# Kernel tuning notes

Measured on AMD Instinct MI355X. Metric: run time of the kernel, lower is better.

The kernel has to match this reference:

```python
import jax, jax.numpy as jnp
import numpy as np


def setup_inputs() -> dict:
    key = jax.random.key(0)
    ks = jax.random.split(key, 24)
    Bz, L, D, U, A, K, V, E, QW = 64, 2048, 512, 512, 512, 64, 32000, 256, 7
    s = 0.02  # weight scale to keep tanh/sigmoid/softmax in a sane range

    def n(k, shape, scale):
        return jax.random.normal(k, shape, dtype=jnp.float32) * scale

    return dict(
        prev_target=n(ks[0], (Bz, V), 0.05),
        prev_hidden=n(ks[1], (Bz, U), 0.05),
        features=n(ks[2], (Bz, L, D), 1.0),
        Bmat=n(ks[3], (Bz, L, 1), 1.0),
        Wa=n(ks[4], (U, A), s),
        Ua=n(ks[5], (D, A), s),
        Va=n(ks[6], (A, 1), s),
        Uf=n(ks[7], (K, A), s),
        Qk=n(ks[8], (QW, 1, K), s),   # Conv1D kernel (W, in_ch=1, out_ch=k)
        We=n(ks[9], (V, E), s),
        Wccz=n(ks[10], (D, U), s),
        Wyz=n(ks[11], (E, U), s),
        Uhz=n(ks[12], (U, U), s),
        Wyr=n(ks[13], (E, U), s),
        Uhr=n(ks[14], (U, U), s),
        Ccr=n(ks[15], (D, U), s),
        Wyh=n(ks[16], (E, U), s),
        b_wyh=jnp.zeros((U,), dtype=jnp.float32),
        Urh=n(ks[17], (U, U), s),
        b_urh=jnp.zeros((U,), dtype=jnp.float32),
        Wo=n(ks[18], (E, V), s),
        Wh=n(ks[19], (U, E), s),
        Wc=n(ks[20], (D, E), s),
    )


def reference(prev_target, prev_hidden, features, Bmat, Wa, Ua, Va, Uf, Qk,
              We, Wccz, Wyz, Uhz, Wyr, Uhr, Ccr, Wyh, b_wyh, Urh, b_urh,
              Wo, Wh, Wc):
    # --- AttentionMLP ---
    # Conv1D(filters=k, kernel_size=q_width, padding='same'), B: (b, L, 1) -> F: (b, L, k)
    F = jax.lax.conv_general_dilated(
        Bmat, Qk, window_strides=(1,), padding='SAME',
        dimension_numbers=('NWC', 'WIO', 'NWC'))
    # e: (b, L, A) = Wa h[:,None,:] + Ua features + Uf F
    e = (prev_hidden @ Wa)[:, None, :] + features @ Ua + F @ Uf
    e = jnp.tanh(e) @ Va                      # (b, L, 1)
    attn = jax.nn.softmax(e, axis=1)          # softmax over L (the reshape trick)
    context = jnp.sum(attn * features, axis=1)  # (b, D)

    # --- GRU-style gating ---
    Ey = prev_target @ We                     # (b, E)
    ccz = context @ Wccz                      # (b, U)
    zt = jax.nn.sigmoid(Ey @ Wyz + prev_hidden @ Uhz + ccz)
    rt = jax.nn.sigmoid(Ey @ Wyr + prev_hidden @ Uhr + context @ Ccr)
    h_cand = jnp.tanh(Ey @ Wyh + b_wyh + (rt * prev_hidden) @ Urh + b_urh + ccz)
    ht = (1.0 - zt) * prev_hidden + zt * h_cand

    # --- Output projection ---
    out = Ey + ht @ Wh + context @ Wc         # (b, E)
    out = jax.nn.softmax(out @ Wo, axis=-1)   # (b, V)
    return out, ht, attn
```

## Files before the change

kernel.cpp:

```cpp
#include <hip/hip_runtime.h>
#include <hip/hip_bf16.h>

typedef unsigned short u16;
typedef __attribute__((ext_vector_type(4))) float f32x4;
typedef __attribute__((ext_vector_type(8))) short bf16x8;

#define BZ 64
#define LSEQ 2048
#define DDIM 512
#define UDIM 512
#define ADIM 512
#define VOC 32000
#define EDIM 256

__device__ __forceinline__ u16 f2bf(float f) {
    union { float f; unsigned int u; } v; v.f = f;
    unsigned int u = v.u;
    return (u16)((u + 0x7FFFu + ((u >> 16) & 1u)) >> 16);
}

__device__ __forceinline__ float fast_tanh(float x) {
    x = fminf(fmaxf(x, -15.f), 15.f);
    float e = __expf(2.f * x);
    return (e - 1.f) * __frcp_rn(e + 1.f);
}

__device__ __forceinline__ void stage16(const u16* __restrict__ g, u16* l, int lane) {
    *(uint4*)(l + lane * 8) = *(const uint4*)g;
}

__global__ void zero_k(float4* p, int n) {
    int i = blockIdx.x * 256 + threadIdx.x;
    if (i < n) { float4 z; z.x = z.y = z.z = z.w = 0.f; p[i] = z; }
}

#define MAXTJ 16
struct TJob { const float* src; u16* dst; int R, C, ld, tileEnd; };
struct TArgs { TJob j[MAXTJ]; int nj; };

__global__ __launch_bounds__(256) void transpose_pack(TArgs a) {
    __shared__ float ts[32][33];
    int bid = blockIdx.x;
    int ji = 0;
    while (bid >= a.j[ji].tileEnd) ji++;
    int tstart = ji ? a.j[ji - 1].tileEnd : 0;
    int local = bid - tstart;
    TJob J = a.j[ji];
    int tilesC = J.C >> 5;
    int tr = local / tilesC, tc = local - tr * tilesC;
    int r0 = tr << 5, c0 = tc << 5;
    int t = threadIdx.x, col = t & 31, row0 = t >> 5;
    #pragma unroll
    for (int i = 0; i < 4; i++) {
        int r = row0 + i * 8;
        ts[r][col] = J.src[(size_t)(r0 + r) * J.C + c0 + col];
    }
    __syncthreads();
    #pragma unroll
    for (int i = 0; i < 4; i++) {
        int crow = row0 + i * 8;
        J.dst[(size_t)(c0 + crow) * J.ld + r0 + col] = f2bf(ts[col][crow]);
    }
}

__global__ void pack_misc(const float* __restrict__ pt, const float* __restrict__ ph,
                          u16* __restrict__ ptb, u16* __restrict__ phb) {
    int idx = blockIdx.x * 256 + threadIdx.x;
    if (idx < BZ * VOC) ptb[idx] = f2bf(pt[idx]);
    int i2 = idx - BZ * VOC;
    if (i2 >= 0 && i2 < BZ * UDIM) phb[i2] = f2bf(ph[i2]);
}

__global__ __launch_bounds__(256) void prep_feat_k(
    const float* __restrict__ feat, const float* __restrict__ Bm,
    const float* __restrict__ Qk, u16* __restrict__ featbf)
{
    __shared__ float qs[448];
    __shared__ float bwin[72];
    int t = threadIdx.x;
    int row0 = blockIdx.x * 64;
    int b = row0 >> 11, l0 = row0 & 2047;
    if (t < 448) qs[t] = Qk[t];
    if (t < 70) { int l = l0 - 3 + t; bwin[t] = (l >= 0 && l < LSEQ) ? Bm[b * LSEQ + l] : 0.f; }
    __syncthreads();
    #pragma unroll
    for (int it = 0; it < 8; it++) {
        int r = it * 8 + (t >> 5), c = (t & 31) * 16;
        const float* p = feat + (size_t)(row0 + r) * DDIM + c;
        float4 a0 = *(const float4*)p, a1 = *(const float4*)(p + 4),
               a2 = *(const float4*)(p + 8), a3 = *(const float4*)(p + 12);
        u16 u[16] = { f2bf(a0.x), f2bf(a0.y), f2bf(a0.z), f2bf(a0.w),
                      f2bf(a1.x), f2bf(a1.y), f2bf(a1.z), f2bf(a1.w),
                      f2bf(a2.x), f2bf(a2.y), f2bf(a2.z), f2bf(a2.w),
                      f2bf(a3.x), f2bf(a3.y), f2bf(a3.z), f2bf(a3.w) };
        u16* dst = featbf + (size_t)(row0 + r) * 576 + c;
        *(uint4*)dst = *(uint4*)u;
        *(uint4*)(dst + 8) = *(uint4*)(u + 8);
    }
    {
        int r = t >> 2, c = (t & 3) * 16;
        float s[16];
        #pragma unroll
        for (int j = 0; j < 16; j++) s[j] = 0.f;
        #pragma unroll
        for (int w7 = 0; w7 < 7; w7++) {
            float bv = bwin[r + w7];
            #pragma unroll
            for (int j = 0; j < 16; j++) s[j] += bv * qs[w7 * 64 + c + j];
        }
        u16 u[16];
        #pragma unroll
        for (int j = 0; j < 16; j++) u[j] = f2bf(s[j]);
        u16* dst = featbf + (size_t)(row0 + r) * 576 + 512 + c;
        *(uint4*)dst = *(uint4*)u;
        *(uint4*)(dst + 8) = *(uint4*)(u + 8);
    }
}

#define MAXGJ 4
struct GJob { const u16* A; const u16* Bt; float* C;
              int ldA, ldB, ldC, nT, ckPer, ckTot, tileEnd, store; };
struct GArgs { GJob j[MAXGJ]; };

__global__ __launch_bounds__(256) void gemm_batch_k(GArgs ga) {
    __shared__ u16 As[64 * 32];
    __shared__ u16 Bs[64 * 32];
    int bid = blockIdx.x, ji = 0;
    while (bid >= ga.j[ji].tileEnd) ji++;
    GJob J = ga.j[ji];
    int local = bid - (ji ? ga.j[ji - 1].tileEnd : 0);
    int nti = local % J.nT, ksi = local / J.nT;
    int n0 = nti * 64;
    int ck0 = ksi * J.ckPer;
    int ckEnd = ck0 + J.ckPer; if (ckEnd > J.ckTot) ckEnd = J.ckTot;
    int tid = threadIdx.x, w = tid >> 6, lane = tid & 63, q = lane >> 4, cc = lane & 15;
    int wrow = lane >> 2, wseg = lane & 3;
    f32x4 acc[4];
    #pragma unroll
    for (int mt = 0; mt < 4; mt++) acc[mt] = (f32x4)0.f;
    const u16* Ab = J.A + (size_t)(w * 16 + wrow) * J.ldA + wseg * 8;
    const u16* Bb = J.Bt + (size_t)(n0 + w * 16 + wrow) * J.ldB + wseg * 8;
    for (int ck = ck0; ck < ckEnd; ck++) {
        int k0 = ck * 32;
        stage16(Ab + k0, &As[w * 512], lane);
        stage16(Bb + k0, &Bs[w * 512], lane);
        __syncthreads();
        bf16x8 af[4];
        #pragma unroll
        for (int mt = 0; mt < 4; mt++)
            af[mt] = *(const bf16x8*)&As[(mt * 16 + cc) * 32 + q * 8];
        bf16x8 bfr = *(const bf16x8*)&Bs[(w * 16 + cc) * 32 + q * 8];
        #pragma unroll
        for (int mt = 0; mt < 4; mt++)
            acc[mt] = __builtin_amdgcn_mfma_f32_16x16x32_bf16(af[mt], bfr, acc[mt], 0, 0, 0);
        __syncthreads();
    }
    #pragma unroll
    for (int mt = 0; mt < 4; mt++) {
        #pragma unroll
        for (int rr = 0; rr < 4; rr++) {
            int m = mt * 16 + q * 4 + rr, n = n0 + w * 16 + cc;
            float v = acc[mt][rr];
            if (J.store) J.C[(size_t)m * J.ldC + n] = v;
            else atomicAdd(&J.C[(size_t)m * J.ldC + n], v);
        }
    }
}

__global__ __launch_bounds__(256) void attn_gemm_k(
    const u16* __restrict__ featbf, const u16* __restrict__ Wt,
    const float* __restrict__ hWa, const float* __restrict__ Va,
    float* __restrict__ e)
{
    __shared__ u16 As[128 * 32];
    __shared__ u16 Bs[128 * 32];
    int row0 = blockIdx.x * 128;
    int col0 = blockIdx.y * 128;
    int b = row0 >> 11;
    int tid = threadIdx.x, w = tid >> 6, lane = tid & 63, q = lane >> 4, cc = lane & 15;
    int wrow = lane >> 2, wseg = lane & 3;
    int rh = w & 1, ch = w >> 1;
    f32x4 acc[4][4];
    #pragma unroll
    for (int mt = 0; mt < 4; mt++)
        #pragma unroll
        for (int nt = 0; nt < 4; nt++) acc[mt][nt] = (f32x4)0.f;
    const u16* Abase = featbf + (size_t)row0 * 576 + wseg * 8;
    const u16* Bbase = Wt + (size_t)col0 * 576 + wseg * 8;
    for (int ck = 0; ck < 18; ck++) {
        int k0 = ck * 32;
        #pragma unroll
        for (int i = 0; i < 2; i++) {
            int rr = (i * 4 + w) * 16 + wrow;
            stage16(Abase + (size_t)rr * 576 + k0, &As[(i * 4 + w) * 512], lane);
            stage16(Bbase + (size_t)rr * 576 + k0, &Bs[(i * 4 + w) * 512], lane);
        }
        __syncthreads();
        bf16x8 af[4], bfr[4];
        #pragma unroll
        for (int mt = 0; mt < 4; mt++)
            af[mt] = *(const bf16x8*)&As[(rh * 64 + mt * 16 + cc) * 32 + q * 8];
        #pragma unroll
        for (int nt = 0; nt < 4; nt++)
            bfr[nt] = *(const bf16x8*)&Bs[(ch * 64 + nt * 16 + cc) * 32 + q * 8];
        #pragma unroll
        for (int mt = 0; mt < 4; mt++)
            #pragma unroll
            for (int nt = 0; nt < 4; nt++)
                acc[mt][nt] = __builtin_amdgcn_mfma_f32_16x16x32_bf16(af[mt], bfr[nt], acc[mt][nt], 0, 0, 0);
        __syncthreads();
    }
    float hv[4], vv[4];
    #pragma unroll
    for (int nt = 0; nt < 4; nt++) {
        int n = col0 + ch * 64 + nt * 16 + cc;
        hv[nt] = hWa[b * ADIM + n];
        vv[nt] = Va[n];
    }
    #pragma unroll
    for (int mt = 0; mt < 4; mt++) {
        #pragma unroll
        for (int rr = 0; rr < 4; rr++) {
            float s = 0.f;
            #pragma unroll
            for (int nt = 0; nt < 4; nt++)
                s += fast_tanh(hv[nt] + acc[mt][nt][rr]) * vv[nt];
            s += __shfl_xor(s, 1, 16);
            s += __shfl_xor(s, 2, 16);
            s += __shfl_xor(s, 4, 16);
            s += __shfl_xor(s, 8, 16);
            if (cc == 0)
                atomicAdd(&e[row0 + rh * 64 + mt * 16 + q * 4 + rr], s);
        }
    }
}

__global__ __launch_bounds__(256) void softmaxL_k(const float* __restrict__ e,
                                                  float* __restrict__ attn_ws,
                                                  float* __restrict__ attn_out) {
    int b = blockIdx.x, t = threadIdx.x;
    __shared__ float sm[4], ss[4];
    float v[8];
    float mx = -1e30f;
    #pragma unroll
    for (int i = 0; i < 8; i++) { v[i] = e[b * LSEQ + t + i * 256]; mx = fmaxf(mx, v[i]); }
    for (int o = 32; o; o >>= 1) mx = fmaxf(mx, __shfl_xor(mx, o, 64));
    if ((t & 63) == 0) sm[t >> 6] = mx;
    __syncthreads();
    mx = fmaxf(fmaxf(sm[0], sm[1]), fmaxf(sm[2], sm[3]));
    float s = 0.f;
    #pragma unroll
    for (int i = 0; i < 8; i++) { v[i] = __expf(v[i] - mx); s += v[i]; }
    for (int o = 32; o; o >>= 1) s += __shfl_xor(s, o, 64);
    if ((t & 63) == 0) ss[t >> 6] = s;
    __syncthreads();
    s = ss[0] + ss[1] + ss[2] + ss[3];
    float inv = 1.f / s;
    #pragma unroll
    for (int i = 0; i < 8; i++) {
        float p = v[i] * inv;
        attn_ws[b * LSEQ + t + i * 256] = p;
        attn_out[b * LSEQ + t + i * 256] = p;
    }
}

__global__ __launch_bounds__(256) void context2_k(
    const u16* __restrict__ featbf, const float* __restrict__ attn,
    float* __restrict__ ctx)
{
    __shared__ float at[256];
    int t = threadIdx.x, b = blockIdx.y, lc = blockIdx.x;
    at[t] = attn[b * LSEQ + lc * 256 + t];
    __syncthreads();
    int col = t * 2;
    const u16* base = featbf + (size_t)(b * LSEQ + lc * 256) * 576 + col;
    float a0 = 0.f, a1 = 0.f;
    #pragma unroll 4
    for (int l = 0; l < 256; l++) {
        unsigned int u = *(const unsigned int*)(base + (size_t)l * 576);
        union { unsigned int i; float f; } lo, hi;
        lo.i = u << 16; hi.i = u & 0xffff0000u;
        float av = at[l];
        a0 += av * lo.f;
        a1 += av * hi.f;
    }
    atomicAdd(&ctx[b * UDIM + col], a0);
    atomicAdd(&ctx[b * UDIM + col + 1], a1);
}

__global__ void pack_acat1_k(const float* __restrict__ Ey, const float* __restrict__ h,
                             const float* __restrict__ ctx, u16* __restrict__ Acat1,
                             const float* __restrict__ bwyh, const float* __restrict__ burh,
                             float* __restrict__ bsum) {
    int b = blockIdx.x, t = threadIdx.x;
    for (int col = t; col < 1280; col += 256) {
        float v = (col < 256) ? Ey[b * 256 + col]
                : (col < 768) ? h[b * 512 + col - 256]
                              : ctx[b * 512 + col - 768];
        Acat1[b * 1280 + col] = f2bf(v);
    }
    if (b == 0) { for (int i = t; i < 512; i += 256) bsum[i] = bwyh[i] + burh[i]; }
}

__global__ void pack_acath_k(const float* __restrict__ Ey, const float* __restrict__ rtp,
                             const float* __restrict__ h, u16* __restrict__ AcatH) {
    int b = blockIdx.x, t = threadIdx.x;
    for (int col = t; col < 768; col += 256) {
        float v;
        if (col < 256) v = Ey[b * 256 + col];
        else {
            int u = col - 256;
            float rt = 1.f / (1.f + __expf(-rtp[b * 512 + u]));
            v = rt * h[b * 512 + u];
        }
        AcatH[b * 768 + col] = f2bf(v);
    }
}

__global__ void pack_ht3_k(const float* __restrict__ ztp, const float* __restrict__ hcp,
                           const float* __restrict__ ccz, const float* __restrict__ bsum,
                           const float* __restrict__ h, const float* __restrict__ ctx,
                           float* __restrict__ ht_out, u16* __restrict__ Acat3) {
    int b = blockIdx.x, t = threadIdx.x;
    for (int u = t; u < 512; u += 256) {
        float z = 1.f / (1.f + __expf(-ztp[b * 512 + u]));
        float hcv = tanhf(hcp[b * 512 + u] + ccz[b * 512 + u] + bsum[u]);
        float v = (1.f - z) * h[b * 512 + u] + z * hcv;
        ht_out[b * 512 + u] = v;
        Acat3[b * 1024 + u] = f2bf(v);
        Acat3[b * 1024 + 512 + u] = f2bf(ctx[b * 512 + u]);
    }
}

__global__ void pack_G_k(const float* __restrict__ Gf32, const float* __restrict__ Ey,
                         u16* __restrict__ Gbf) {
    int b = blockIdx.x, t = threadIdx.x;
    Gbf[b * 256 + t] = f2bf(Gf32[b * 256 + t] + Ey[b * 256 + t]);
}

__global__ __launch_bounds__(1024) void softmaxV_k(const float* __restrict__ logits,
                                                   float* __restrict__ out) {
    int b = blockIdx.x, t = threadIdx.x;
    __shared__ float sm[16], ss[16];
    const float* lp = logits + (size_t)b * VOC;
    float mx = -1e30f;
    for (int i = t; i < VOC; i += 1024) mx = fmaxf(mx, lp[i]);
    for (int o = 32; o; o >>= 1) mx = fmaxf(mx, __shfl_xor(mx, o, 64));
    if ((t & 63) == 0) sm[t >> 6] = mx;
    __syncthreads();
    if (t < 16) {
        float m2 = sm[t];
        for (int o = 8; o; o >>= 1) m2 = fmaxf(m2, __shfl_xor(m2, o, 16));
        sm[t] = m2;
    }
    __syncthreads();
    mx = sm[0];
    float s = 0.f;
    for (int i = t; i < VOC; i += 1024) s += __expf(lp[i] - mx);
    for (int o = 32; o; o >>= 1) s += __shfl_xor(s, o, 64);
    if ((t & 63) == 0) ss[t >> 6] = s;
    __syncthreads();
    if (t < 16) {
        float s2 = ss[t];
        for (int o = 8; o; o >>= 1) s2 += __shfl_xor(s2, o, 16);
        ss[t] = s2;
    }
    __syncthreads();
    float inv = 1.f / ss[0];
    float* op = out + (size_t)b * VOC;
    for (int i = t; i < VOC; i += 1024) op[i] = __expf(lp[i] - mx) * inv;
}

#define OFF_FEATBF ((size_t)0)
#define OFF_WTCAT  ((size_t)150994944)
#define OFF_WTWA   ((size_t)151584768)
#define OFF_WTWE   ((size_t)152109056)
#define OFF_WTWO   ((size_t)168493056)
#define OFF_WTHC   ((size_t)184877056)
#define OFF_WTZ    ((size_t)185401344)
#define OFF_WTR    ((size_t)186712064)
#define OFF_WTH    ((size_t)188022784)
#define OFF_PTB    ((size_t)188809216)
#define OFF_PHB    ((size_t)192905216)
#define OFF_E      ((size_t)192970752)
#define OFF_HWA    ((size_t)193495040)
#define OFF_EY     ((size_t)193626112)
#define OFF_CTX    ((size_t)193691648)
#define OFF_ZTP    ((size_t)193822720)
#define OFF_RTP    ((size_t)193953792)
#define OFF_CCZ    ((size_t)194084864)
#define OFF_HCP    ((size_t)194215936)
#define OFF_GF32   ((size_t)194347008)
#define OFF_ATTNWS ((size_t)194412544)
#define OFF_ACAT1  ((size_t)194936832)
#define OFF_ACATH  ((size_t)195100672)
#define OFF_ACAT3  ((size_t)195198976)
#define OFF_BSUM   ((size_t)195330048)
#define OFF_GBF    ((size_t)195332096)
#define OFF_LOGITS OFF_FEATBF

extern "C" void kernel_launch(void* const* d_in, const int* in_sizes, int n_in,
                              void* d_out, int out_size, void* d_ws, size_t ws_size,
                              hipStream_t stream)
{
    const float* prev_target = (const float*)d_in[0];
    const float* prev_hidden = (const float*)d_in[1];
    const float* features    = (const float*)d_in[2];
    const float* Bmat        = (const float*)d_in[3];
    const float* Wa    = (const float*)d_in[4];
    const float* Ua    = (const float*)d_in[5];
    const float* Va    = (const float*)d_in[6];
    const float* Uf    = (const float*)d_in[7];
    const float* Qk    = (const float*)d_in[8];
    const float* We    = (const float*)d_in[9];
    const float* Wccz  = (const float*)d_in[10];
    const float* Wyz   = (const float*)d_in[11];
    const float* Uhz   = (const float*)d_in[12];
    const float* Wyr   = (const float*)d_in[13];
    const float* Uhr   = (const float*)d_in[14];
    const float* Ccr   = (const float*)d_in[15];
    const float* Wyh   = (const float*)d_in[16];
    const float* b_wyh = (const float*)d_in[17];
    const float* Urh   = (const float*)d_in[18];
    const float* b_urh = (const float*)d_in[19];
    const float* Wo    = (const float*)d_in[20];
    const float* Wh    = (const float*)d_in[21];
    const float* Wc    = (const float*)d_in[22];

    char* w = (char*)d_ws;
    u16*   featbf  = (u16*)(w + OFF_FEATBF);
    u16*   Wt_cat  = (u16*)(w + OFF_WTCAT);
    u16*   Wt_wa   = (u16*)(w + OFF_WTWA);
    u16*   Wt_we   = (u16*)(w + OFF_WTWE);
    u16*   Wt_wo   = (u16*)(w + OFF_WTWO);
    u16*   Wt_hc   = (u16*)(w + OFF_WTHC);
    u16*   Wt_z    = (u16*)(w + OFF_WTZ);
    u16*   Wt_r    = (u16*)(w + OFF_WTR);
    u16*   Wt_h    = (u16*)(w + OFF_WTH);
    u16*   pt_bf   = (u16*)(w + OFF_PTB);
    u16*   ph_bf   = (u16*)(w + OFF_PHB);
    float* e_buf   = (float*)(w + OFF_E);
    float* hWa_buf = (float*)(w + OFF_HWA);
    float* Ey_buf  = (float*)(w + OFF_EY);
    float* ctx_buf = (float*)(w + OFF_CTX);
    float* ztp_buf = (float*)(w + OFF_ZTP);
    float* rtp_buf = (float*)(w + OFF_RTP);
    float* ccz_buf = (float*)(w + OFF_CCZ);
    float* hcp_buf = (float*)(w + OFF_HCP);
    float* Gf32    = (float*)(w + OFF_GF32);
    float* attn_ws = (float*)(w + OFF_ATTNWS);
    u16*   Acat1   = (u16*)(w + OFF_ACAT1);
    u16*   AcatH   = (u16*)(w + OFF_ACATH);
    u16*   Acat3   = (u16*)(w + OFF_ACAT3);
    float* bsum    = (float*)(w + OFF_BSUM);
    u16*   Gbf     = (u16*)(w + OFF_GBF);
    float* logits  = (float*)(w + OFF_LOGITS);

    float* out      = (float*)d_out;
    float* ht_out   = out + (size_t)BZ * VOC;
    float* attn_out = ht_out + (size_t)BZ * UDIM;

    TArgs ta;
    int cum = 0, ji = 0;
    auto addJob = [&](const float* src, u16* dst, int R, int C, int ld) {
        cum += (R / 32) * (C / 32);
        ta.j[ji].src = src; ta.j[ji].dst = dst;
        ta.j[ji].R = R; ta.j[ji].C = C; ta.j[ji].ld = ld; ta.j[ji].tileEnd = cum;
        ji++;
    };
    addJob(Ua,   Wt_cat + 0,   512, 512, 576);
    addJob(Uf,   Wt_cat + 512,  64, 512, 576);
    addJob(Wa,   Wt_wa,        512, 512, 512);
    addJob(We,   Wt_we,      32000, 256, 32000);
    addJob(Wo,   Wt_wo,        256, 32000, 256);
    addJob(Wh,   Wt_hc + 0,    512, 256, 1024);
    addJob(Wc,   Wt_hc + 512,  512, 256, 1024);
    addJob(Wyz,  Wt_z + 0,     256, 512, 1280);
    addJob(Uhz,  Wt_z + 256,   512, 512, 1280);
    addJob(Wccz, Wt_z + 768,   512, 512, 1280);
    addJob(Wyr,  Wt_r + 0,     256, 512, 1280);
    addJob(Uhr,  Wt_r + 256,   512, 512, 1280);
    addJob(Ccr,  Wt_r + 768,   512, 512, 1280);
    addJob(Wyh,  Wt_h + 0,     256, 512, 768);
    addJob(Urh,  Wt_h + 256,   512, 512, 768);
    ta.nj = ji;

    auto mkjob = [](const u16* A, int ldA, const u16* Bt, int ldB, float* C, int ldC,
                    int N, int K, int ckPer, int& c2) {
        GJob g; g.A = A; g.Bt = Bt; g.C = C; g.ldA = ldA; g.ldB = ldB; g.ldC = ldC;
        g.nT = N / 64; g.ckTot = K / 32; g.ckPer = ckPer;
        int ks = (g.ckTot + ckPer - 1) / ckPer;
        c2 += g.nT * ks; g.tileEnd = c2;
        g.store = (ckPer >= g.ckTot) ? 1 : 0;
        return g;
    };

    hipLaunchKernelGGL(zero_k, dim3(352), dim3(256), 0, stream, (float4*)e_buf, 90112);
    hipLaunchKernelGGL(transpose_pack, dim3(cum), dim3(256), 0, stream, ta);
    hipLaunchKernelGGL(pack_misc, dim3(8128), dim3(256), 0, stream,
                       prev_target, prev_hidden, pt_bf, ph_bf);
    hipLaunchKernelGGL(prep_feat_k, dim3(2048), dim3(256), 0, stream,
                       features, Bmat, Qk, featbf);
    {
        GArgs ga; int c2 = 0;
        ga.j[0] = mkjob(ph_bf, 512, Wt_wa, 512, hWa_buf, 512, 512, 512, 4, c2);
        ga.j[1] = mkjob(pt_bf, 32000, Wt_we, 32000, Ey_buf, 256, 256, 32000, 20, c2);
        hipLaunchKernelGGL(gemm_batch_k, dim3(c2), dim3(256), 0, stream, ga);
    }
    hipLaunchKernelGGL(attn_gemm_k, dim3(1024, 4), dim3(256), 0, stream,
                       featbf, Wt_cat, hWa_buf, Va, e_buf);
    hipLaunchKernelGGL(softmaxL_k, dim3(64), dim3(256), 0, stream, e_buf, attn_ws, attn_out);
    hipLaunchKernelGGL(context2_k, dim3(8, 64), dim3(256), 0, stream,
                       featbf, attn_ws, ctx_buf);
    hipLaunchKernelGGL(pack_acat1_k, dim3(64), dim3(256), 0, stream,
                       Ey_buf, prev_hidden, ctx_buf, Acat1, b_wyh, b_urh, bsum);
    {
        GArgs ga; int c2 = 0;
        ga.j[0] = mkjob(Acat1, 1280, Wt_z, 1280, ztp_buf, 512, 512, 1280, 8, c2);
        ga.j[1] = mkjob(Acat1, 1280, Wt_r, 1280, rtp_buf, 512, 512, 1280, 8, c2);
        ga.j[2] = mkjob(Acat1 + 768, 1280, Wt_z + 768, 1280, ccz_buf, 512, 512, 512, 4, c2);
        hipLaunchKernelGGL(gemm_batch_k, dim3(c2), dim3(256), 0, stream, ga);
    }
    hipLaunchKernelGGL(pack_acath_k, dim3(64), dim3(256), 0, stream,
                       Ey_buf, rtp_buf, prev_hidden, AcatH);
    {
        GArgs ga; int c2 = 0;
        ga.j[0] = mkjob(AcatH, 768, Wt_h, 768, hcp_buf, 512, 512, 768, 6, c2);
        hipLaunchKernelGGL(gemm_batch_k, dim3(c2), dim3(256), 0, stream, ga);
    }
    hipLaunchKernelGGL(pack_ht3_k, dim3(64), dim3(256), 0, stream,
                       ztp_buf, hcp_buf, ccz_buf, bsum, prev_hidden, ctx_buf, ht_out, Acat3);
    {
        GArgs ga; int c2 = 0;
        ga.j[0] = mkjob(Acat3, 1024, Wt_hc, 1024, Gf32, 256, 256, 1024, 8, c2);
        hipLaunchKernelGGL(gemm_batch_k, dim3(c2), dim3(256), 0, stream, ga);
    }
    hipLaunchKernelGGL(pack_G_k, dim3(64), dim3(256), 0, stream, Gf32, Ey_buf, Gbf);
    {
        GArgs ga; int c2 = 0;
        ga.j[0] = mkjob(Gbf, 256, Wt_wo, 256, logits, 32000, 32000, 256, 8, c2);
        hipLaunchKernelGGL(gemm_batch_k, dim3(c2), dim3(256), 0, stream, ga);
    }
    hipLaunchKernelGGL(softmaxV_k, dim3(64), dim3(1024), 0, stream, logits, out);
}
```

Before: 726.5 us.

## Fuse GRU pack kernels into GEMM A-tile staging and epilogues

Removes the four small pack kernels: the GEMM now builds its bf16 A tile on the fly from Ey/h/ctx, the sigmoid-gated hidden state, or the computed ht, and writes ht_out and the Ey-added bf16 G output from its staging and epilogue. Shared-memory tiles are padded from 32 to 40 elements per row, presumably to avoid LDS bank conflicts. The attention GEMM grid is flattened with a block-index swizzle, and some split-K factors change (hWa and the final hc GEMM become single-pass stores). This cuts launches and intermediate buffer round-trips, at the cost of redundant per-tile recomputation of activations (tanh/sigmoid recomputed for every N-tile and split).

```diff
diff --git a/kernel.cpp b/kernel.cpp
--- a/kernel.cpp
+++ b/kernel.cpp
@@ -25,8 +25,8 @@
     return (e - 1.f) * __frcp_rn(e + 1.f);
 }
 
-__device__ __forceinline__ void stage16(const u16* __restrict__ g, u16* l, int lane) {
-    *(uint4*)(l + lane * 8) = *(const uint4*)g;
+__device__ __forceinline__ float fast_sig(float x) {
+    return 1.f / (1.f + __expf(-x));
 }
 
 __global__ void zero_k(float4* p, int n) {
@@ -119,15 +119,17 @@
 
 #define MAXGJ 4
 struct GJob { const u16* A; const u16* Bt; float* C;
-              int ldA, ldB, ldC, nT, ckPer, ckTot, tileEnd, store; };
-struct GArgs { GJob j[MAXGJ]; };
+              int ldA, ldB, ldC, nT, ckPer, ckTot, tileEnd, koff, mode, epi; };
+struct GAux { const float *Ey, *h, *ctx, *rtp, *ztp, *hcp, *ccz, *bwyh, *burh; float* ht_out; };
+struct GArgs { GJob j[MAXGJ]; GAux x; };
 
 __global__ __launch_bounds__(256) void gemm_batch_k(GArgs ga) {
-    __shared__ u16 As[64 * 32];
-    __shared__ u16 Bs[64 * 32];
+    __shared__ u16 As[64 * 40];
+    __shared__ u16 Bs[64 * 40];
     int bid = blockIdx.x, ji = 0;
     while (bid >= ga.j[ji].tileEnd) ji++;
     GJob J = ga.j[ji];
+    GAux x = ga.x;
     int local = bid - (ji ? ga.j[ji - 1].tileEnd : 0);
     int nti = local % J.nT, ksi = local / J.nT;
     int n0 = nti * 64;
@@ -135,21 +137,56 @@
     int ckEnd = ck0 + J.ckPer; if (ckEnd > J.ckTot) ckEnd = J.ckTot;
     int tid = threadIdx.x, w = tid >> 6, lane = tid & 63, q = lane >> 4, cc = lane & 15;
     int wrow = lane >> 2, wseg = lane & 3;
+    int m = w * 16 + wrow;
     f32x4 acc[4];
     #pragma unroll
     for (int mt = 0; mt < 4; mt++) acc[mt] = (f32x4)0.f;
-    const u16* Ab = J.A + (size_t)(w * 16 + wrow) * J.ldA + wseg * 8;
-    const u16* Bb = J.Bt + (size_t)(n0 + w * 16 + wrow) * J.ldB + wseg * 8;
+    const u16* Ab = (J.mode == 0) ? (J.A + (size_t)m * J.ldA + wseg * 8) : nullptr;
+    const u16* Bb = J.Bt + (size_t)(n0 + m) * J.ldB + wseg * 8;
     for (int ck = ck0; ck < ckEnd; ck++) {
         int k0 = ck * 32;
-        stage16(Ab + k0, &As[w * 512], lane);
-        stage16(Bb + k0, &Bs[w * 512], lane);
+        if (J.mode == 0) {
+            *(uint4*)&As[m * 40 + wseg * 8] = *(const uint4*)(Ab + k0);
+        } else {
+            int cbase = J.koff + k0 + wseg * 8;
+            u16 gen[8];
+            #pragma unroll
+            for (int jj = 0; jj < 8; jj++) {
+                int c = cbase + jj;
+                float v;
+                if (J.mode == 1) {
+                    v = (c < 256) ? x.Ey[m * 256 + c]
+                      : (c < 768) ? x.h[m * 512 + c - 256]
+                                  : x.ctx[m * 512 + c - 768];
+                } else if (J.mode == 2) {
+                    if (c < 256) v = x.Ey[m * 256 + c];
+                    else {
+                        int u = c - 256;
+                        v = fast_sig(x.rtp[m * 512 + u]) * x.h[m * 512 + u];
+                    }
+                } else {
+                    if (c < 512) {
+                        int u = c;
+                        float z = fast_sig(x.ztp[m * 512 + u]);
+                        float hc = tanhf(x.hcp[m * 512 + u] + x.ccz[m * 512 + u]
+                                         + x.bwyh[u] + x.burh[u]);
+                        v = (1.f - z) * x.h[m * 512 + u] + z * hc;
+                        if (n0 == 0) x.ht_out[m * 512 + u] = v;
+                    } else {
+                        v = x.ctx[m * 512 + c - 512];
+                    }
+                }
+                gen[jj] = f2bf(v);
+            }
+            *(uint4*)&As[m * 40 + wseg * 8] = *(uint4*)gen;
+        }
+        *(uint4*)&Bs[m * 40 + wseg * 8] = *(const uint4*)(Bb + k0);
         __syncthreads();
         bf16x8 af[4];
         #pragma unroll
         for (int mt = 0; mt < 4; mt++)
-            af[mt] = *(const bf16x8*)&As[(mt * 16 + cc) * 32 + q * 8];
-        bf16x8 bfr = *(const bf16x8*)&Bs[(w * 16 + cc) * 32 + q * 8];
+            af[mt] = *(const bf16x8*)&As[(mt * 16 + cc) * 40 + q * 8];
+        bf16x8 bfr = *(const bf16x8*)&Bs[(w * 16 + cc) * 40 + q * 8];
         #pragma unroll
         for (int mt = 0; mt < 4; mt++)
             acc[mt] = __builtin_amdgcn_mfma_f32_16x16x32_bf16(af[mt], bfr, acc[mt], 0, 0, 0);
@@ -159,10 +196,11 @@
     for (int mt = 0; mt < 4; mt++) {
         #pragma unroll
         for (int rr = 0; rr < 4; rr++) {
-            int m = mt * 16 + q * 4 + rr, n = n0 + w * 16 + cc;
+            int mm = mt * 16 + q * 4 + rr, n = n0 + w * 16 + cc;
             float v = acc[mt][rr];
-            if (J.store) J.C[(size_t)m * J.ldC + n] = v;
-            else atomicAdd(&J.C[(size_t)m * J.ldC + n], v);
+            if (J.epi == 0) atomicAdd(&J.C[(size_t)mm * J.ldC + n], v);
+            else if (J.epi == 1) J.C[(size_t)mm * J.ldC + n] = v;
+            else ((u16*)J.C)[(size_t)mm * J.ldC + n] = f2bf(v + x.Ey[mm * 256 + n]);
         }
     }
 }
@@ -172,10 +210,12 @@
     const float* __restrict__ hWa, const float* __restrict__ Va,
     float* __restrict__ e)
 {
-    __shared__ u16 As[128 * 32];
-    __shared__ u16 Bs[128 * 32];
-    int row0 = blockIdx.x * 128;
-    int col0 = blockIdx.y * 128;
+    __shared__ u16 As[128 * 40];
+    __shared__ u16 Bs[128 * 40];
+    int bid = blockIdx.x;
+    int job = (bid & 7) * 512 + (bid >> 3);
+    int row0 = (job >> 2) * 128;
+    int col0 = (job & 3) * 128;
     int b = row0 >> 11;
     int tid = threadIdx.x, w = tid >> 6, lane = tid & 63, q = lane >> 4, cc = lane & 15;
     int wrow = lane >> 2, wseg = lane & 3;
@@ -192,17 +232,17 @@
         #pragma unroll
         for (int i = 0; i < 2; i++) {
             int rr = (i * 4 + w) * 16 + wrow;
-            stage16(Abase + (size_t)rr * 576 + k0, &As[(i * 4 + w) * 512], lane);
-            stage16(Bbase + (size_t)rr * 576 + k0, &Bs[(i * 4 + w) * 512], lane);
+            *(uint4*)&As[rr * 40 + wseg * 8] = *(const uint4*)(Abase + (size_t)rr * 576 + k0);
+            *(uint4*)&Bs[rr * 40 + wseg * 8] = *(const uint4*)(Bbase + (size_t)rr * 576 + k0);
         }
         __syncthreads();
         bf16x8 af[4], bfr[4];
         #pragma unroll
         for (int mt = 0; mt < 4; mt++)
-            af[mt] = *(const bf16x8*)&As[(rh * 64 + mt * 16 + cc) * 32 + q * 8];
+            af[mt] = *(const bf16x8*)&As[(rh * 64 + mt * 16 + cc) * 40 + q * 8];
         #pragma unroll
         for (int nt = 0; nt < 4; nt++)
-            bfr[nt] = *(const bf16x8*)&Bs[(ch * 64 + nt * 16 + cc) * 32 + q * 8];
+            bfr[nt] = *(const bf16x8*)&Bs[(ch * 64 + nt * 16 + cc) * 40 + q * 8];
         #pragma unroll
         for (int mt = 0; mt < 4; mt++)
             #pragma unroll
@@ -286,56 +326,6 @@
     }
     atomicAdd(&ctx[b * UDIM + col], a0);
     atomicAdd(&ctx[b * UDIM + col + 1], a1);
-}
-
-__global__ void pack_acat1_k(const float* __restrict__ Ey, const float* __restrict__ h,
-                             const float* __restrict__ ctx, u16* __restrict__ Acat1,
-                             const float* __restrict__ bwyh, const float* __restrict__ burh,
-                             float* __restrict__ bsum) {
-    int b = blockIdx.x, t = threadIdx.x;
-    for (int col = t; col < 1280; col += 256) {
-        float v = (col < 256) ? Ey[b * 256 + col]
-                : (col < 768) ? h[b * 512 + col - 256]
-                              : ctx[b * 512 + col - 768];
-        Acat1[b * 1280 + col] = f2bf(v);
-    }
-    if (b == 0) { for (int i = t; i < 512; i += 256) bsum[i] = bwyh[i] + burh[i]; }
-}
-
-__global__ void pack_acath_k(const float* __restrict__ Ey, const float* __restrict__ rtp,
-                             const float* __restrict__ h, u16* __restrict__ AcatH) {
-    int b = blockIdx.x, t = threadIdx.x;
-    for (int col = t; col < 768; col += 256) {
-        float v;
-        if (col < 256) v = Ey[b * 256 + col];
-        else {
-            int u = col - 256;
-            float rt = 1.f / (1.f + __expf(-rtp[b * 512 + u]));
-            v = rt * h[b * 512 + u];
-        }
-        AcatH[b * 768 + col] = f2bf(v);
-    }
-}
-
-__global__ void pack_ht3_k(const float* __restrict__ ztp, const float* __restrict__ hcp,
-                           const float* __restrict__ ccz, const float* __restrict__ bsum,
-                           const float* __restrict__ h, const float* __restrict__ ctx,
-                           float* __restrict__ ht_out, u16* __restrict__ Acat3) {
-    int b = blockIdx.x, t = threadIdx.x;
-    for (int u = t; u < 512; u += 256) {
-        float z = 1.f / (1.f + __expf(-ztp[b * 512 + u]));
-        float hcv = tanhf(hcp[b * 512 + u] + ccz[b * 512 + u] + bsum[u]);
-        float v = (1.f - z) * h[b * 512 + u] + z * hcv;
-        ht_out[b * 512 + u] = v;
-        Acat3[b * 1024 + u] = f2bf(v);
-        Acat3[b * 1024 + 512 + u] = f2bf(ctx[b * 512 + u]);
-    }
-}
-
-__global__ void pack_G_k(const float* __restrict__ Gf32, const float* __restrict__ Ey,
-                         u16* __restrict__ Gbf) {
-    int b = blockIdx.x, t = threadIdx.x;
-    Gbf[b * 256 + t] = f2bf(Gf32[b * 256 + t] + Ey[b * 256 + t]);
 }
 
 __global__ __launch_bounds__(1024) void softmaxV_k(const float* __restrict__ logits,
@@ -390,13 +380,8 @@
 #define OFF_RTP    ((size_t)193953792)
 #define OFF_CCZ    ((size_t)194084864)
 #define OFF_HCP    ((size_t)194215936)
-#define OFF_GF32   ((size_t)194347008)
-#define OFF_ATTNWS ((size_t)194412544)
-#define OFF_ACAT1  ((size_t)194936832)
-#define OFF_ACATH  ((size_t)195100672)
-#define OFF_ACAT3  ((size_t)195198976)
-#define OFF_BSUM   ((size_t)195330048)
-#define OFF_GBF    ((size_t)195332096)
+#define OFF_ATTNWS ((size_t)194347008)
+#define OFF_GBF    ((size_t)194871296)
 #define OFF_LOGITS OFF_FEATBF
 
 extern "C" void kernel_launch(void* const* d_in, const int* in_sizes, int n_in,
@@ -447,12 +432,7 @@
     float* rtp_buf = (float*)(w + OFF_RTP);
     float* ccz_buf = (float*)(w + OFF_CCZ);
     float* hcp_buf = (float*)(w + OFF_HCP);
-    float* Gf32    = (float*)(w + OFF_GF32);
     float* attn_ws = (float*)(w + OFF_ATTNWS);
-    u16*   Acat1   = (u16*)(w + OFF_ACAT1);
-    u16*   AcatH   = (u16*)(w + OFF_ACATH);
-    u16*   Acat3   = (u16*)(w + OFF_ACAT3);
-    float* bsum    = (float*)(w + OFF_BSUM);
     u16*   Gbf     = (u16*)(w + OFF_GBF);
     float* logits  = (float*)(w + OFF_LOGITS);
 
@@ -485,60 +465,58 @@
     addJob(Urh,  Wt_h + 256,   512, 512, 768);
     ta.nj = ji;
 
+    GAux aux;
+    aux.Ey = Ey_buf; aux.h = prev_hidden; aux.ctx = ctx_buf;
+    aux.rtp = rtp_buf; aux.ztp = ztp_buf; aux.hcp = hcp_buf; aux.ccz = ccz_buf;
+    aux.bwyh = b_wyh; aux.burh = b_urh; aux.ht_out = ht_out;
+
     auto mkjob = [](const u16* A, int ldA, const u16* Bt, int ldB, float* C, int ldC,
-                    int N, int K, int ckPer, int& c2) {
+                    int N, int K, int ckPer, int koff, int mode, int epi, int& c2) {
         GJob g; g.A = A; g.Bt = Bt; g.C = C; g.ldA = ldA; g.ldB = ldB; g.ldC = ldC;
         g.nT = N / 64; g.ckTot = K / 32; g.ckPer = ckPer;
+        g.koff = koff; g.mode = mode; g.epi = epi;
         int ks = (g.ckTot + ckPer - 1) / ckPer;
         c2 += g.nT * ks; g.tileEnd = c2;
-        g.store = (ckPer >= g.ckTot) ? 1 : 0;
         return g;
     };
 
-    hipLaunchKernelGGL(zero_k, dim3(352), dim3(256), 0, stream, (float4*)e_buf, 90112);
+    hipLaunchKernelGGL(zero_k, dim3(336), dim3(256), 0, stream, (float4*)e_buf, 86016);
     hipLaunchKernelGGL(transpose_pack, dim3(cum), dim3(256), 0, stream, ta);
     hipLaunchKernelGGL(pack_misc, dim3(8128), dim3(256), 0, stream,
                        prev_target, prev_hidden, pt_bf, ph_bf);
     hipLaunchKernelGGL(prep_feat_k, dim3(2048), dim3(256), 0, stream,
                        features, Bmat, Qk, featbf);
     {
-        GArgs ga; int c2 = 0;
-        ga.j[0] = mkjob(ph_bf, 512, Wt_wa, 512, hWa_buf, 512, 512, 512, 4, c2);
-        ga.j[1] = mkjob(pt_bf, 32000, Wt_we, 32000, Ey_buf, 256, 256, 32000, 20, c2);
+        GArgs ga; ga.x = aux; int c2 = 0;
+        ga.j[0] = mkjob(ph_bf, 512, Wt_wa, 512, hWa_buf, 512, 512, 512, 16, 0, 0, 1, c2);
+        ga.j[1] = mkjob(pt_bf, 32000, Wt_we, 32000, Ey_buf, 256, 256, 32000, 20, 0, 0, 0, c2);
         hipLaunchKernelGGL(gemm_batch_k, dim3(c2), dim3(256), 0, stream, ga);
     }
-    hipLaunchKernelGGL(attn_gemm_k, dim3(1024, 4), dim3(256), 0, stream,
+    hipLaunchKernelGGL(attn_gemm_k, dim3(4096), dim3(256), 0, stream,
                        featbf, Wt_cat, hWa_buf, Va, e_buf);
     hipLaunchKernelGGL(softmaxL_k, dim3(64), dim3(256), 0, stream, e_buf, attn_ws, attn_out);
     hipLaunchKernelGGL(context2_k, dim3(8, 64), dim3(256), 0, stream,
                        featbf, attn_ws, ctx_buf);
-    hipLaunchKernelGGL(pack_acat1_k, dim3(64), dim3(256), 0, stream,
-                       Ey_buf, prev_hidden, ctx_buf, Acat1, b_wyh, b_urh, bsum);
     {
-        GArgs ga; int c2 = 0;
-        ga.j[0] = mkjob(Acat1, 1280, Wt_z, 1280, ztp_buf, 512, 512, 1280, 8, c2);
-        ga.j[1] = mkjob(Acat1, 1280, Wt_r, 1280, rtp_buf, 512, 512, 1280, 8, c2);
-        ga.j[2] = mkjob(Acat1 + 768, 1280, Wt_z + 768, 1280, ccz_buf, 512, 512, 512, 4, c2);
+        GArgs ga; ga.x = aux; int c2 = 0;
+        ga.j[0] = mkjob(nullptr, 0, Wt_z, 1280, ztp_buf, 512, 512, 1280, 8, 0, 1, 0, c2);
+        ga.j[1] = mkjob(nullptr, 0, Wt_r, 1280, rtp_buf, 512, 512, 1280, 8, 0, 1, 0, c2);
+        ga.j[2] = mkjob(nullptr, 0, Wt_z + 768, 1280, ccz_buf, 512, 512, 512, 8, 768, 1, 0, c2);
         hipLaunchKernelGGL(gemm_batch_k, dim3(c2), dim3(256), 0, stream, ga);
     }
-    hipLaunchKernelGGL(pack_acath_k, dim3(64), dim3(256), 0, stream,
-                       Ey_buf, rtp_buf, prev_hidden, AcatH);
     {
-        GArgs ga; int c2 = 0;
-        ga.j[0] = mkjob(AcatH, 768, Wt_h, 768, hcp_buf, 512, 512, 768, 6, c2);
+        GArgs ga; ga.x = aux; int c2 = 0;
+        ga.j[0] = mkjob(nullptr, 0, Wt_h, 768, hcp_buf, 512, 512, 768, 8, 0, 2, 0, c2);
         hipLaunchKernelGGL(gemm_batch_k, dim3(c2), dim3(256), 0, stream, ga);
     }
-    hipLaunchKernelGGL(pack_ht3_k, dim3(64), dim3(256), 0, stream,
-                       ztp_buf, hcp_buf, ccz_buf, bsum, prev_hidden, ctx_buf, ht_out, Acat3);
     {
-        GArgs ga; int c2 = 0;
-        ga.j[0] = mkjob(Acat3, 1024, Wt_hc, 1024, Gf32, 256, 256, 1024, 8, c2);
+        GArgs ga; ga.x = aux; int c2 = 0;
+        ga.j[0] = mkjob(nullptr, 0, Wt_hc, 1024, (float*)Gbf, 256, 256, 1024, 32, 0, 3, 2, c2);
         hipLaunchKernelGGL(gemm_batch_k, dim3(c2), dim3(256), 0, stream, ga);
     }
-    hipLaunchKernelGGL(pack_G_k, dim3(64), dim3(256), 0, stream, Gf32, Ey_buf, Gbf);
     {
-        GArgs ga; int c2 = 0;
-        ga.j[0] = mkjob(Gbf, 256, Wt_wo, 256, logits, 32000, 32000, 256, 8, c2);
+        GArgs ga; ga.x = aux; int c2 = 0;
+        ga.j[0] = mkjob(Gbf, 256, Wt_wo, 256, logits, 32000, 32000, 256, 8, 0, 0, 1, c2);
         hipLaunchKernelGGL(gemm_batch_k, dim3(c2), dim3(256), 0, stream, ga);
     }
     hipLaunchKernelGGL(softmaxV_k, dim3(64), dim3(1024), 0, stream, logits, out);
```

Measured after the change: 879.1 us. 1.21x slower.

## Prefetch-pipeline attention GEMM with padded LDS, remapped grid, finer split-K

Applied to the files above, without the earlier changes.

The attention GEMM now stages K-chunks of 64 instead of 32. The next chunk's global loads are prefetched into registers while MFMAs run on the current one. Shared tiles are padded (stride 72/40) to avoid LDS bank conflicts, and the grid is flattened with a block-index remap so neighbouring blocks share operand tiles in cache. The small batched GEMMs also get their LDS padded and smaller split-K chunk sizes, which means more blocks and more atomics. Register pressure goes up because of the prefetch buffers.

```diff
diff --git a/kernel.cpp b/kernel.cpp
--- a/kernel.cpp
+++ b/kernel.cpp
@@ -23,10 +23,6 @@
     x = fminf(fmaxf(x, -15.f), 15.f);
     float e = __expf(2.f * x);
     return (e - 1.f) * __frcp_rn(e + 1.f);
-}
-
-__device__ __forceinline__ void stage16(const u16* __restrict__ g, u16* l, int lane) {
-    *(uint4*)(l + lane * 8) = *(const uint4*)g;
 }
 
 __global__ void zero_k(float4* p, int n) {
@@ -123,8 +119,8 @@
 struct GArgs { GJob j[MAXGJ]; };
 
 __global__ __launch_bounds__(256) void gemm_batch_k(GArgs ga) {
-    __shared__ u16 As[64 * 32];
-    __shared__ u16 Bs[64 * 32];
+    __shared__ u16 As[64 * 40];
+    __shared__ u16 Bs[64 * 40];
     int bid = blockIdx.x, ji = 0;
     while (bid >= ga.j[ji].tileEnd) ji++;
     GJob J = ga.j[ji];
@@ -135,21 +131,22 @@
     int ckEnd = ck0 + J.ckPer; if (ckEnd > J.ckTot) ckEnd = J.ckTot;
     int tid = threadIdx.x, w = tid >> 6, lane = tid & 63, q = lane >> 4, cc = lane & 15;
     int wrow = lane >> 2, wseg = lane & 3;
+    int m = w * 16 + wrow;
     f32x4 acc[4];
     #pragma unroll
     for (int mt = 0; mt < 4; mt++) acc[mt] = (f32x4)0.f;
-    const u16* Ab = J.A + (size_t)(w * 16 + wrow) * J.ldA + wseg * 8;
-    const u16* Bb = J.Bt + (size_t)(n0 + w * 16 + wrow) * J.ldB + wseg * 8;
+    const u16* Ab = J.A + (size_t)m * J.ldA + wseg * 8;
+    const u16* Bb = J.Bt + (size_t)(n0 + m) * J.ldB + wseg * 8;
     for (int ck = ck0; ck < ckEnd; ck++) {
         int k0 = ck * 32;
-        stage16(Ab + k0, &As[w * 512], lane);
-        stage16(Bb + k0, &Bs[w * 512], lane);
+        *(uint4*)&As[m * 40 + wseg * 8] = *(const uint4*)(Ab + k0);
+        *(uint4*)&Bs[m * 40 + wseg * 8] = *(const uint4*)(Bb + k0);
         __syncthreads();
         bf16x8 af[4];
         #pragma unroll
         for (int mt = 0; mt < 4; mt++)
-            af[mt] = *(const bf16x8*)&As[(mt * 16 + cc) * 32 + q * 8];
-        bf16x8 bfr = *(const bf16x8*)&Bs[(w * 16 + cc) * 32 + q * 8];
+            af[mt] = *(const bf16x8*)&As[(mt * 16 + cc) * 40 + q * 8];
+        bf16x8 bfr = *(const bf16x8*)&Bs[(w * 16 + cc) * 40 + q * 8];
         #pragma unroll
         for (int mt = 0; mt < 4; mt++)
             acc[mt] = __builtin_amdgcn_mfma_f32_16x16x32_bf16(af[mt], bfr, acc[mt], 0, 0, 0);
@@ -159,10 +156,10 @@
     for (int mt = 0; mt < 4; mt++) {
         #pragma unroll
         for (int rr = 0; rr < 4; rr++) {
-            int m = mt * 16 + q * 4 + rr, n = n0 + w * 16 + cc;
+            int mm = mt * 16 + q * 4 + rr, n = n0 + w * 16 + cc;
             float v = acc[mt][rr];
-            if (J.store) J.C[(size_t)m * J.ldC + n] = v;
-            else atomicAdd(&J.C[(size_t)m * J.ldC + n], v);
+            if (J.store) J.C[(size_t)mm * J.ldC + n] = v;
+            else atomicAdd(&J.C[(size_t)mm * J.ldC + n], v);
         }
     }
 }
@@ -172,43 +169,61 @@
     const float* __restrict__ hWa, const float* __restrict__ Va,
     float* __restrict__ e)
 {
-    __shared__ u16 As[128 * 32];
-    __shared__ u16 Bs[128 * 32];
-    int row0 = blockIdx.x * 128;
-    int col0 = blockIdx.y * 128;
+    __shared__ u16 As[128 * 72];
+    __shared__ u16 Bs[128 * 72];
+    int bid = blockIdx.x;
+    int job = (bid & 7) * 512 + (bid >> 3);
+    int row0 = (job >> 2) * 128;
+    int col0 = (job & 3) * 128;
     int b = row0 >> 11;
     int tid = threadIdx.x, w = tid >> 6, lane = tid & 63, q = lane >> 4, cc = lane & 15;
-    int wrow = lane >> 2, wseg = lane & 3;
     int rh = w & 1, ch = w >> 1;
+    int srow = tid >> 3, sseg = tid & 7;
+    const u16* Ag = featbf + (size_t)(row0 + srow) * 576 + sseg * 8;
+    const u16* Bg = Wt + (size_t)(col0 + srow) * 576 + sseg * 8;
+    uint4 pa[4], pb[4];
+    #pragma unroll
+    for (int p = 0; p < 4; p++) {
+        pa[p] = *(const uint4*)(Ag + (size_t)p * 32 * 576);
+        pb[p] = *(const uint4*)(Bg + (size_t)p * 32 * 576);
+    }
     f32x4 acc[4][4];
     #pragma unroll
     for (int mt = 0; mt < 4; mt++)
         #pragma unroll
         for (int nt = 0; nt < 4; nt++) acc[mt][nt] = (f32x4)0.f;
-    const u16* Abase = featbf + (size_t)row0 * 576 + wseg * 8;
-    const u16* Bbase = Wt + (size_t)col0 * 576 + wseg * 8;
-    for (int ck = 0; ck < 18; ck++) {
-        int k0 = ck * 32;
-        #pragma unroll
-        for (int i = 0; i < 2; i++) {
-            int rr = (i * 4 + w) * 16 + wrow;
-            stage16(Abase + (size_t)rr * 576 + k0, &As[(i * 4 + w) * 512], lane);
-            stage16(Bbase + (size_t)rr * 576 + k0, &Bs[(i * 4 + w) * 512], lane);
+
+    for (int ck = 0; ck < 9; ck++) {
+        if (ck) __syncthreads();
+        #pragma unroll
+        for (int p = 0; p < 4; p++) {
+            *(uint4*)&As[(srow + p * 32) * 72 + sseg * 8] = pa[p];
+            *(uint4*)&Bs[(srow + p * 32) * 72 + sseg * 8] = pb[p];
         }
         __syncthreads();
-        bf16x8 af[4], bfr[4];
-        #pragma unroll
-        for (int mt = 0; mt < 4; mt++)
-            af[mt] = *(const bf16x8*)&As[(rh * 64 + mt * 16 + cc) * 32 + q * 8];
-        #pragma unroll
-        for (int nt = 0; nt < 4; nt++)
-            bfr[nt] = *(const bf16x8*)&Bs[(ch * 64 + nt * 16 + cc) * 32 + q * 8];
-        #pragma unroll
-        for (int mt = 0; mt < 4; mt++)
+        if (ck < 8) {
+            int k0 = (ck + 1) * 64;
+            #pragma unroll
+            for (int p = 0; p < 4; p++) {
+                pa[p] = *(const uint4*)(Ag + (size_t)p * 32 * 576 + k0);
+                pb[p] = *(const uint4*)(Bg + (size_t)p * 32 * 576 + k0);
+            }
+        }
+        #pragma unroll
+        for (int kk = 0; kk < 2; kk++) {
+            bf16x8 af[4], bfr[4];
+            #pragma unroll
+            for (int mt = 0; mt < 4; mt++)
+                af[mt] = *(const bf16x8*)&As[(rh * 64 + mt * 16 + cc) * 72 + kk * 32 + q * 8];
             #pragma unroll
             for (int nt = 0; nt < 4; nt++)
-                acc[mt][nt] = __builtin_amdgcn_mfma_f32_16x16x32_bf16(af[mt], bfr[nt], acc[mt][nt], 0, 0, 0);
-        __syncthreads();
+                bfr[nt] = *(const bf16x8*)&Bs[(ch * 64 + nt * 16 + cc) * 72 + kk * 32 + q * 8];
+            #pragma unroll
+            for (int mt = 0; mt < 4; mt++)
+                #pragma unroll
+                for (int nt = 0; nt < 4; nt++)
+                    acc[mt][nt] = __builtin_amdgcn_mfma_f32_16x16x32_bf16(af[mt], bfr[nt], acc[mt][nt], 0, 0, 0);
+        }
     }
     float hv[4], vv[4];
     #pragma unroll
@@ -504,10 +519,10 @@
     {
         GArgs ga; int c2 = 0;
         ga.j[0] = mkjob(ph_bf, 512, Wt_wa, 512, hWa_buf, 512, 512, 512, 4, c2);
-        ga.j[1] = mkjob(pt_bf, 32000, Wt_we, 32000, Ey_buf, 256, 256, 32000, 20, c2);
+        ga.j[1] = mkjob(pt_bf, 32000, Wt_we, 32000, Ey_buf, 256, 256, 32000, 10, c2);
         hipLaunchKernelGGL(gemm_batch_k, dim3(c2), dim3(256), 0, stream, ga);
     }
-    hipLaunchKernelGGL(attn_gemm_k, dim3(1024, 4), dim3(256), 0, stream,
+    hipLaunchKernelGGL(attn_gemm_k, dim3(4096), dim3(256), 0, stream,
                        featbf, Wt_cat, hWa_buf, Va, e_buf);
     hipLaunchKernelGGL(softmaxL_k, dim3(64), dim3(256), 0, stream, e_buf, attn_ws, attn_out);
     hipLaunchKernelGGL(context2_k, dim3(8, 64), dim3(256), 0, stream,
@@ -516,8 +531,8 @@
                        Ey_buf, prev_hidden, ctx_buf, Acat1, b_wyh, b_urh, bsum);
     {
         GArgs ga; int c2 = 0;
-        ga.j[0] = mkjob(Acat1, 1280, Wt_z, 1280, ztp_buf, 512, 512, 1280, 8, c2);
-        ga.j[1] = mkjob(Acat1, 1280, Wt_r, 1280, rtp_buf, 512, 512, 1280, 8, c2);
+        ga.j[0] = mkjob(Acat1, 1280, Wt_z, 1280, ztp_buf, 512, 512, 1280, 5, c2);
+        ga.j[1] = mkjob(Acat1, 1280, Wt_r, 1280, rtp_buf, 512, 512, 1280, 5, c2);
         ga.j[2] = mkjob(Acat1 + 768, 1280, Wt_z + 768, 1280, ccz_buf, 512, 512, 512, 4, c2);
         hipLaunchKernelGGL(gemm_batch_k, dim3(c2), dim3(256), 0, stream, ga);
     }
@@ -525,14 +540,14 @@
                        Ey_buf, rtp_buf, prev_hidden, AcatH);
     {
         GArgs ga; int c2 = 0;
-        ga.j[0] = mkjob(AcatH, 768, Wt_h, 768, hcp_buf, 512, 512, 768, 6, c2);
+        ga.j[0] = mkjob(AcatH, 768, Wt_h, 768, hcp_buf, 512, 512, 768, 3, c2);
         hipLaunchKernelGGL(gemm_batch_k, dim3(c2), dim3(256), 0, stream, ga);
     }
     hipLaunchKernelGGL(pack_ht3_k, dim3(64), dim3(256), 0, stream,
                        ztp_buf, hcp_buf, ccz_buf, bsum, prev_hidden, ctx_buf, ht_out, Acat3);
     {
         GArgs ga; int c2 = 0;
-        ga.j[0] = mkjob(Acat3, 1024, Wt_hc, 1024, Gf32, 256, 256, 1024, 8, c2);
+        ga.j[0] = mkjob(Acat3, 1024, Wt_hc, 1024, Gf32, 256, 256, 1024, 4, c2);
         hipLaunchKernelGGL(gemm_batch_k, dim3(c2), dim3(256), 0, stream, ga);
     }
     hipLaunchKernelGGL(pack_G_k, dim3(64), dim3(256), 0, stream, Gf32, Ey_buf, Gbf);
```

Measured after the change: 1.152 ms. 1.59x slower.
